# Kernel optimization log

Measured on AMD Instinct MI355X. Metric: run time of the kernel, lower is better.

Reference implementation:

```python
import jax, jax.numpy as jnp
import numpy as np

B, S, D, H = 4, 2048, 1024, 16
DK = D // H


def setup_inputs() -> dict:
    key = jax.random.key(0)
    ks = jax.random.split(key, 9)
    sc = 1.0 / np.sqrt(D)
    return {
        "query": jax.random.normal(ks[0], (B, S, D), jnp.float32),
        "key": jax.random.normal(ks[1], (B, S, D), jnp.float32),
        "value": jax.random.normal(ks[2], (B, S, D), jnp.float32),
        "Wq": jax.random.normal(ks[3], (D, D), jnp.float32) * sc,
        "bq": jax.random.normal(ks[4], (D,), jnp.float32) * sc,
        "Wk": jax.random.normal(ks[5], (D, D), jnp.float32) * sc,
        "bk": jax.random.normal(ks[6], (D,), jnp.float32) * sc,
        "Wv": jax.random.normal(ks[7], (D, D), jnp.float32) * sc,
        "bv": jax.random.normal(ks[8], (D,), jnp.float32) * sc,
    }


def reference(query, key, value, Wq, bq, Wk, bk, Wv, bv):
    # QKV projections, split into heads: [B,S,D] -> [B,H,S,DK]
    q = (query @ Wq + bq).reshape(B, S, H, DK).transpose(0, 2, 1, 3)
    k = (key @ Wk + bk).reshape(B, S, H, DK).transpose(0, 2, 1, 3)
    v = (value @ Wv + bv).reshape(B, S, H, DK).transpose(0, 2, 1, 3)
    # NOTE: original module applies NO 1/sqrt(d_k) scaling
    attn = jnp.einsum("bhqd,bhkd->bhqk", q, k)
    attn = jax.nn.softmax(attn, axis=-1)  # dropout is identity at inference
    ctx = jnp.einsum("bhqk,bhkd->bhqd", attn, v)
    ctx = ctx.transpose(0, 2, 1, 3).reshape(B, S, D)
    # original adds residual to raw concatenated context (no output projection)
    return ctx + query
```

## Files before the change

### kernel.cpp

```cpp
#include <hip/hip_runtime.h>
#include <hip/hip_bf16.h>
#include <stdint.h>

#define Bb 4
#define Ss 2048
#define Dd 1024
#define Hh 16
#define DK 64
#define BH 64
#define Mm 8192
#define KVT 64

typedef __attribute__((ext_vector_type(8))) _Float16 f16x8;
typedef __attribute__((ext_vector_type(4))) _Float16 f16x4;
typedef __attribute__((ext_vector_type(2))) __fp16 fp16x2;
typedef __attribute__((ext_vector_type(4))) float f32x4;
typedef __attribute__((ext_vector_type(16))) float f32x16;
typedef __attribute__((ext_vector_type(2))) unsigned uint2v;

__device__ __forceinline__ void gload16(const _Float16* g, _Float16* lds) {
  __builtin_amdgcn_global_load_lds((const __attribute__((address_space(1))) unsigned int*)g,
                                   (__attribute__((address_space(3))) unsigned int*)lds, 16, 0, 0);
}

#if __has_builtin(__builtin_amdgcn_exp2f)
__device__ __forceinline__ float ex2(float x) { return __builtin_amdgcn_exp2f(x); }
#else
__device__ __forceinline__ float ex2(float x) {
  float r; asm("v_exp_f32 %0, %1" : "=v"(r) : "v"(x)); return r;
}
#endif

__device__ __forceinline__ unsigned pk2u(float a, float b) {
  union { fp16x2 h; unsigned u; } x;
  x.h = __builtin_amdgcn_cvt_pkrtz(a, b);
  return x.u;
}

__device__ __forceinline__ float xhalf_max(float x) {
  union { float f; unsigned u; } a; a.f = x;
  uint2v r = __builtin_amdgcn_permlane32_swap(a.u, a.u, false, false);
  union { unsigned u; float f; } b0, b1; b0.u = r[0]; b1.u = r[1];
  return fmaxf(fmaxf(x, b0.f), b1.f);
}

__global__ __launch_bounds__(256) void cvt_wt(const float* __restrict__ wq,
                                              const float* __restrict__ wk,
                                              const float* __restrict__ wv,
                                              _Float16* __restrict__ tq,
                                              _Float16* __restrict__ tk,
                                              _Float16* __restrict__ tv) {
  const float* w = blockIdx.z == 0 ? wq : (blockIdx.z == 1 ? wk : wv);
  _Float16* o = blockIdx.z == 0 ? tq : (blockIdx.z == 1 ? tk : tv);
  float wscale = blockIdx.z == 0 ? 1.4426950408889634f : 1.0f;
  __shared__ float tile[64][65];
  int k0 = blockIdx.x * 64;
  int n0 = blockIdx.y * 64;
  int t = threadIdx.x;
  int tr = t >> 4;
  int tc = (t & 15) * 4;
  for (int i = 0; i < 4; i++) {
    int r = i * 16 + tr;
    float4 val = *(const float4*)(w + (k0 + r) * Dd + n0 + tc);
    tile[r][tc + 0] = val.x; tile[r][tc + 1] = val.y;
    tile[r][tc + 2] = val.z; tile[r][tc + 3] = val.w;
  }
  __syncthreads();
  for (int i = 0; i < 2; i++) {
    int vdx = t + 256 * i;
    int rn = vdx >> 3;
    int c8 = (vdx & 7) * 8;
    union { f16x8 v8; _Float16 h[8]; } o2;
    for (int j = 0; j < 8; j++) o2.h[j] = (_Float16)(tile[c8 + j][rn] * wscale);
    *(f16x8*)(o + (n0 + rn) * Dd + k0 + c8) = o2.v8;
  }
}

__global__ __launch_bounds__(256) void gemm_qkv(
    const float* __restrict__ aq, const float* __restrict__ ak,
    const float* __restrict__ av,
    const _Float16* __restrict__ wtq, const _Float16* __restrict__ wtk,
    const _Float16* __restrict__ wtv,
    const float* __restrict__ bq, const float* __restrict__ bk, const float* __restrict__ bv,
    _Float16* __restrict__ oq, _Float16* __restrict__ ok,
    _Float16* __restrict__ ov) {
  int z = blockIdx.z;
  const float* Af    = z == 0 ? aq  : (z == 1 ? ak  : av);
  const _Float16* Bt = z == 0 ? wtq : (z == 1 ? wtk : wtv);
  const float* bias  = z == 0 ? bq  : (z == 1 ? bk  : bv);
  _Float16* out      = z == 0 ? oq  : (z == 1 ? ok  : ov);
  float bscale       = z == 0 ? 1.4426950408889634f : 1.0f;

  __shared__ _Float16 As[2][128 * 64];
  __shared__ _Float16 Bs[2][128 * 64];

  int tid = threadIdx.x;
  int w = tid >> 6;
  int l = tid & 63;
  int lr = l & 15, lk = l >> 4;
  int m0 = blockIdx.x * 128;
  int n0 = blockIdx.y * 128;
  int wr = (w >> 1) * 64;
  int wc = (w & 1) * 64;

  int srow = l >> 3;
  int cs = (l & 7) ^ srow;
  const float*    ap[4];
  const _Float16* bp[4];
#pragma unroll
  for (int i = 0; i < 4; i++) {
    int row = i * 32 + w * 8 + srow;
    ap[i] = Af + (size_t)(m0 + row) * Dd + cs * 8;
    bp[i] = Bt + (size_t)(n0 + row) * Dd + cs * 8;
  }

  f32x4 acc[4][4] = {};
  int lr7 = lr & 7;
  int rs0 = (lk ^ lr7) * 8;
  int rs1 = ((4 + lk) ^ lr7) * 8;

#define ALOAD(AR)                                                         \
  _Pragma("unroll")                                                       \
  for (int i = 0; i < 4; i++) {                                           \
    AR[i][0] = *(const float4*)(ap[i]);                                   \
    AR[i][1] = *(const float4*)(ap[i] + 4);                               \
    ap[i] += 64;                                                          \
  }
#define BDMA(NXT)                                                         \
  _Pragma("unroll")                                                       \
  for (int i = 0; i < 4; i++) {                                           \
    gload16(bp[i], &Bs[NXT][(i * 256 + w * 64) * 8]);                     \
    bp[i] += 64;                                                          \
  }
#define AWRITE(AR, NXT)                                                   \
  _Pragma("unroll")                                                       \
  for (int i = 0; i < 4; i++) {                                           \
    union { unsigned u[4]; f16x8 v; } aw;                                 \
    aw.u[0] = pk2u(AR[i][0].x, AR[i][0].y);                               \
    aw.u[1] = pk2u(AR[i][0].z, AR[i][0].w);                               \
    aw.u[2] = pk2u(AR[i][1].x, AR[i][1].y);                               \
    aw.u[3] = pk2u(AR[i][1].z, AR[i][1].w);                               \
    *(f16x8*)&As[NXT][(i * 256 + w * 64 + l) * 8] = aw.v;                 \
  }
#define GCOMP(CUR)                                                              \
  _Pragma("unroll")                                                             \
  for (int kh = 0; kh < 2; kh++) {                                              \
    int rs = kh ? rs1 : rs0;                                                    \
    f16x8 af[4], bf[4];                                                         \
    _Pragma("unroll")                                                           \
    for (int mi = 0; mi < 4; mi++)                                              \
      af[mi] = *(const f16x8*)&As[CUR][(wr + mi * 16 + lr) * 64 + rs];          \
    _Pragma("unroll")                                                           \
    for (int ni = 0; ni < 4; ni++)                                              \
      bf[ni] = *(const f16x8*)&Bs[CUR][(wc + ni * 16 + lr) * 64 + rs];          \
    _Pragma("unroll")                                                           \
    for (int mi = 0; mi < 4; mi++)                                              \
      _Pragma("unroll")                                                         \
      for (int ni = 0; ni < 4; ni++)                                            \
        acc[mi][ni] = __builtin_amdgcn_mfma_f32_16x16x32_f16(af[mi], bf[ni], acc[mi][ni], 0, 0, 0); \
  }

  {
    float4 ar[4][2];
    ALOAD(ar)
    BDMA(0)
    AWRITE(ar, 0)
  }
  __syncthreads();

  for (int it = 0; it < 7; ++it) {
    {
      float4 ar[4][2];
      ALOAD(ar)
      BDMA(1)
      GCOMP(0)
      AWRITE(ar, 1)
    }
    __syncthreads();
    {
      float4 ar[4][2];
      ALOAD(ar)
      BDMA(0)
      GCOMP(1)
      AWRITE(ar, 0)
    }
    __syncthreads();
  }
  {
    float4 ar[4][2];
    ALOAD(ar)
    BDMA(1)
    GCOMP(0)
    AWRITE(ar, 1)
  }
  __syncthreads();
  GCOMP(1)
#undef GCOMP
#undef AWRITE
#undef BDMA
#undef ALOAD

  if (z == 2) {
    for (int mi = 0; mi < 4; mi++) {
      for (int ni = 0; ni < 4; ni++) {
        int n = n0 + wc + ni * 16 + lr;
        float bval = bias[n];
        int h = n >> 6, dk = n & 63;
        int m = m0 + wr + mi * 16 + lk * 4;
        int b = m >> 11, s = m & 2047;
        f16x4 o4;
        for (int j = 0; j < 4; j++) o4[j] = (_Float16)(acc[mi][ni][j] + bval);
        *(f16x4*)(out + ((size_t)((b * Hh + h) * DK + dk) * Ss + s)) = o4;
      }
    }
  } else {
    for (int mi = 0; mi < 4; mi++) {
      for (int ni = 0; ni < 4; ni++) {
        int n = n0 + wc + ni * 16 + lr;
        float bval = bias[n] * bscale;
        int h = n >> 6, dk = n & 63;
        for (int j = 0; j < 4; j++) {
          int m = m0 + wr + mi * 16 + lk * 4 + j;
          int b = m >> 11, s = m & 2047;
          out[((b * Hh + h) * Ss + s) * DK + dk] = (_Float16)(acc[mi][ni][j] + bval);
        }
      }
    }
  }
}

__global__ __launch_bounds__(256) void attn(const _Float16* __restrict__ Qb,
                                            const _Float16* __restrict__ Kb,
                                            const _Float16* __restrict__ Vt,
                                            const float* __restrict__ query,
                                            float* __restrict__ outp) {
  __shared__ _Float16 Kl[2][KVT * 64];
  __shared__ _Float16 Vl[2][KVT * 64];

  int tid = threadIdx.x;
  int w = tid >> 6, l = tid & 63;
  int l31 = l & 31, hi = l >> 5;
  int bh = blockIdx.x;
  int q0 = blockIdx.y * 128 + w * 32;
  const _Float16* Qp = Qb + bh * (Ss * DK);
  const _Float16* Kp = Kb + bh * (Ss * DK);
  const _Float16* Vp = Vt + bh * (DK * Ss);

  int srow = l >> 3;
  int sslot = (l & 7) ^ (srow & 7);
  int w16 = w * 16;
  const _Float16* kp0 = Kp + (w16 + srow) * DK + sslot * 8;
  const _Float16* kp1 = Kp + (w16 + 8 + srow) * DK + sslot * 8;
  const _Float16* vp0 = Vp + (w16 + srow) * Ss + sslot * 8;
  const _Float16* vp1 = Vp + (w16 + 8 + srow) * Ss + sslot * 8;

#define STAGE(BUF)                                                        \
  {                                                                       \
    gload16(kp0, &Kl[BUF][w16 * 64]);                                     \
    gload16(kp1, &Kl[BUF][(w16 + 8) * 64]);                               \
    gload16(vp0, &Vl[BUF][w16 * 64]);                                     \
    gload16(vp1, &Vl[BUF][(w16 + 8) * 64]);                               \
    kp0 += KVT * DK; kp1 += KVT * DK; vp0 += KVT; vp1 += KVT;             \
  }

  f16x8 qf[4];
#pragma unroll
  for (int s = 0; s < 4; s++)
    qf[s] = *(const f16x8*)(Qp + (q0 + l31) * DK + s * 16 + hi * 8);

  f32x16 o0 = {}, o1 = {};
  float mrun = -1e30f, lrun = 0.f;

  int kv7 = l31 & 7;
  int rslot[4];
#pragma unroll
  for (int s = 0; s < 4; s++) rslot[s] = ((s * 2 + hi) ^ kv7) * 8;

#define TILE(BUF)                                                               \
  {                                                                             \
    f32x16 s0 = {}, s1 = {};                                                    \
    _Pragma("unroll")                                                           \
    for (int s = 0; s < 4; s++) {                                               \
      f16x8 ka = *(const f16x8*)&Kl[BUF][l31 * 64 + rslot[s]];                  \
      s0 = __builtin_amdgcn_mfma_f32_32x32x16_f16(ka, qf[s], s0, 0, 0, 0);      \
    }                                                                           \
    _Pragma("unroll")                                                           \
    for (int s = 0; s < 4; s++) {                                               \
      f16x8 kb = *(const f16x8*)&Kl[BUF][(32 + l31) * 64 + rslot[s]];           \
      s1 = __builtin_amdgcn_mfma_f32_32x32x16_f16(kb, qf[s], s1, 0, 0, 0);      \
    }                                                                           \
    float m8[8];                                                                \
    _Pragma("unroll")                                                           \
    for (int r = 0; r < 8; r++)                                                 \
      m8[r] = fmaxf(fmaxf(s0[r], s0[r + 8]), fmaxf(s1[r], s1[r + 8]));          \
    _Pragma("unroll")                                                           \
    for (int d = 4; d >= 1; d >>= 1)                                            \
      for (int r = 0; r < 4; r++) if (r < d) m8[r] = fmaxf(m8[r], m8[r + d]);   \
    float pm = xhalf_max(m8[0]);                                                \
    if (!__all(pm - mrun <= 8.f)) {            \
      float mn = fmaxf(mrun, pm);                                               \
      float sc_ = ex2(mrun - mn);                                               \
      mrun = mn;                                                                \
      lrun *= sc_;                                                              \
      _Pragma("unroll")                                                         \
      for (int r = 0; r < 16; r++) { o0[r] *= sc_; o1[r] *= sc_; }              \
    }                                                                           \
    _Pragma("unroll")                                                           \
    for (int r = 0; r < 16; r++) {                                              \
      s0[r] = ex2(s0[r] - mrun);                                                \
      s1[r] = ex2(s1[r] - mrun);                                                \
    }                                                                           \
    float s8[8];                                                                \
    _Pragma("unroll")                                                           \
    for (int r = 0; r < 8; r++) s8[r] = (s0[r] + s0[r + 8]) + (s1[r] + s1[r + 8]); \
    _Pragma("unroll")                                                           \
    for (int d = 4; d >= 1; d >>= 1)                                            \
      for (int r = 0; r < 4; r++) if (r < d) s8[r] += s8[r + d];                \
    lrun += s8[0];                                                              \
    PVSTEP(BUF, s0, 0, 0)                                                       \
    PVSTEP(BUF, s0, 8, 1)                                                       \
    PVSTEP(BUF, s1, 0, 2)                                                       \
    PVSTEP(BUF, s1, 8, 3)                                                       \
  }

#define PVSTEP(BUF, SRC, OFF, KST)                                              \
    {                                                                           \
      unsigned a0 = pk2u(SRC[(OFF) + 0], SRC[(OFF) + 1]);                       \
      unsigned a1 = pk2u(SRC[(OFF) + 2], SRC[(OFF) + 3]);                       \
      unsigned b0 = pk2u(SRC[(OFF) + 4], SRC[(OFF) + 5]);                       \
      unsigned b1 = pk2u(SRC[(OFF) + 6], SRC[(OFF) + 7]);                       \
      uint2v r0 = __builtin_amdgcn_permlane32_swap(a0, b0, false, false);       \
      uint2v r1 = __builtin_amdgcn_permlane32_swap(a1, b1, false, false);       \
      union { unsigned u[4]; f16x8 v; } pf;                                     \
      pf.u[0] = r0[0]; pf.u[1] = r1[0]; pf.u[2] = r0[1]; pf.u[3] = r1[1];       \
      f16x8 v0 = *(const f16x8*)&Vl[BUF][l31 * 64 + rslot[KST]];                \
      f16x8 v1 = *(const f16x8*)&Vl[BUF][(32 + l31) * 64 + rslot[KST]];         \
      o0 = __builtin_amdgcn_mfma_f32_32x32x16_f16(v0, pf.v, o0, 0, 0, 0);       \
      o1 = __builtin_amdgcn_mfma_f32_32x32x16_f16(v1, pf.v, o1, 0, 0, 0);       \
    }

  STAGE(0)
  __syncthreads();

  for (int it = 0; it < 15; ++it) {
    STAGE(1)
    TILE(0)
    __syncthreads();
    STAGE(0)
    TILE(1)
    __syncthreads();
  }
  STAGE(1)
  TILE(0)
  __syncthreads();
  TILE(1)
#undef PVSTEP
#undef TILE
#undef STAGE

  lrun += __shfl_xor(lrun, 32);
  int b = bh >> 4, h = bh & 15;
  float inv = 1.f / lrun;
  int base = (b * Ss + q0 + l31) * Dd + h * 64;
#pragma unroll
  for (int rq = 0; rq < 4; rq++) {
    int d0 = rq * 8 + hi * 4;
    float4 qv0 = *(const float4*)(query + base + d0);
    float4 ov0;
    ov0.x = o0[rq * 4 + 0] * inv + qv0.x;
    ov0.y = o0[rq * 4 + 1] * inv + qv0.y;
    ov0.z = o0[rq * 4 + 2] * inv + qv0.z;
    ov0.w = o0[rq * 4 + 3] * inv + qv0.w;
    *(float4*)(outp + base + d0) = ov0;
    float4 qv1 = *(const float4*)(query + base + 32 + d0);
    float4 ov1;
    ov1.x = o1[rq * 4 + 0] * inv + qv1.x;
    ov1.y = o1[rq * 4 + 1] * inv + qv1.y;
    ov1.z = o1[rq * 4 + 2] * inv + qv1.z;
    ov1.w = o1[rq * 4 + 3] * inv + qv1.w;
    *(float4*)(outp + base + 32 + d0) = ov1;
  }
}

extern "C" void kernel_launch(void* const* d_in, const int* in_sizes, int n_in,
                              void* d_out, int out_size, void* d_ws, size_t ws_size,
                              hipStream_t stream) {
  const float* query = (const float*)d_in[0];
  const float* key   = (const float*)d_in[1];
  const float* value = (const float*)d_in[2];
  const float* Wq = (const float*)d_in[3];
  const float* bq = (const float*)d_in[4];
  const float* Wk = (const float*)d_in[5];
  const float* bk = (const float*)d_in[6];
  const float* Wv = (const float*)d_in[7];
  const float* bv = (const float*)d_in[8];
  float* out = (float*)d_out;

  _Float16* ws = (_Float16*)d_ws;
  const size_t ACT = (size_t)Mm * Dd;
  const size_t WSZ = (size_t)Dd * Dd;
  _Float16* Wtq  = ws;
  _Float16* Wtk  = Wtq + WSZ;
  _Float16* Wtv  = Wtk + WSZ;
  _Float16* Qb   = Wtv + WSZ;
  _Float16* Kb   = Qb + ACT;
  _Float16* VtT  = Kb + ACT;

  cvt_wt<<<dim3(16, 16, 3), dim3(256), 0, stream>>>(Wq, Wk, Wv, Wtq, Wtk, Wtv);
  gemm_qkv<<<dim3(64, 8, 3), dim3(256), 0, stream>>>(query, key, value, Wtq, Wtk, Wtv,
                                                     bq, bk, bv, Qb, Kb, VtT);
  attn<<<dim3(64, 16), dim3(256), 0, stream>>>(Qb, Kb, VtT, query, out);
}
```

Baseline: 195.4 us.

## Restructure attention into single-wave blocks with vmcnt-based double buffering

The attention kernel now runs one wave per block on 32 query rows and streams 32-key K/V tiles into double-buffered LDS. Each wave loads its own tiles, so the block-wide barriers give way to explicit s_waitcnt vmcnt waits. s_setprio is raised around the MFMA sections. This drops cross-wave synchronisation, but each wave now loads all of K/V alone, with no sharing across four waves, so global/L2 traffic for K/V roughly quadruples and occupancy depends on many small blocks.

After: 230.1 us. +17.8%, slower.

```diff
diff --git a/kernel.cpp b/kernel.cpp
--- a/kernel.cpp
+++ b/kernel.cpp
@@ -9,7 +9,6 @@
 #define DK 64
 #define BH 64
 #define Mm 8192
-#define KVT 64
 
 typedef __attribute__((ext_vector_type(8))) _Float16 f16x8;
 typedef __attribute__((ext_vector_type(4))) _Float16 f16x4;
@@ -43,6 +42,12 @@
   union { unsigned u; float f; } b0, b1; b0.u = r[0]; b1.u = r[1];
   return fmaxf(fmaxf(x, b0.f), b1.f);
 }
+
+#define VW(N)                                                           \
+  do {                                                                  \
+    asm volatile("s_waitcnt vmcnt(" #N ")" ::: "memory");               \
+    __builtin_amdgcn_sched_barrier(0);                                  \
+  } while (0)
 
 __global__ __launch_bounds__(256) void cvt_wt(const float* __restrict__ wq,
                                               const float* __restrict__ wk,
@@ -229,38 +234,43 @@
   }
 }
 
-__global__ __launch_bounds__(256) void attn(const _Float16* __restrict__ Qb,
-                                            const _Float16* __restrict__ Kb,
-                                            const _Float16* __restrict__ Vt,
-                                            const float* __restrict__ query,
-                                            float* __restrict__ outp) {
-  __shared__ _Float16 Kl[2][KVT * 64];
-  __shared__ _Float16 Vl[2][KVT * 64];
-
-  int tid = threadIdx.x;
-  int w = tid >> 6, l = tid & 63;
+__global__ __launch_bounds__(64) void attn(const _Float16* __restrict__ Qb,
+                                           const _Float16* __restrict__ Kb,
+                                           const _Float16* __restrict__ Vt,
+                                           const float* __restrict__ query,
+                                           float* __restrict__ outp) {
+  __shared__ _Float16 Kl[2][32 * 64];
+  __shared__ _Float16 Vl[2][64 * 32];
+
+  int l = threadIdx.x;
   int l31 = l & 31, hi = l >> 5;
   int bh = blockIdx.x;
-  int q0 = blockIdx.y * 128 + w * 32;
+  int q0 = blockIdx.y * 32;
   const _Float16* Qp = Qb + bh * (Ss * DK);
   const _Float16* Kp = Kb + bh * (Ss * DK);
   const _Float16* Vp = Vt + bh * (DK * Ss);
 
-  int srow = l >> 3;
-  int sslot = (l & 7) ^ (srow & 7);
-  int w16 = w * 16;
-  const _Float16* kp0 = Kp + (w16 + srow) * DK + sslot * 8;
-  const _Float16* kp1 = Kp + (w16 + 8 + srow) * DK + sslot * 8;
-  const _Float16* vp0 = Vp + (w16 + srow) * Ss + sslot * 8;
-  const _Float16* vp1 = Vp + (w16 + 8 + srow) * Ss + sslot * 8;
-
-#define STAGE(BUF)                                                        \
+  int kr = l >> 3;
+  int kcs = (l & 7) ^ kr;
+  const _Float16* kpA = Kp + (kr + 0)  * DK + kcs * 8;
+  const _Float16* kpB = Kp + (kr + 8)  * DK + kcs * 8;
+  const _Float16* kpC = Kp + (kr + 16) * DK + kcs * 8;
+  const _Float16* kpD = Kp + (kr + 24) * DK + kcs * 8;
+  int vr = l >> 2;
+  int vcs = (l & 3) ^ ((l >> 3) & 3);
+  const _Float16* vpA = Vp + (vr + 0)  * Ss + vcs * 8;
+  const _Float16* vpB = Vp + (vr + 16) * Ss + vcs * 8;
+  const _Float16* vpC = Vp + (vr + 32) * Ss + vcs * 8;
+  const _Float16* vpD = Vp + (vr + 48) * Ss + vcs * 8;
+
+#define STAGE(B)                                                          \
   {                                                                       \
-    gload16(kp0, &Kl[BUF][w16 * 64]);                                     \
-    gload16(kp1, &Kl[BUF][(w16 + 8) * 64]);                               \
-    gload16(vp0, &Vl[BUF][w16 * 64]);                                     \
-    gload16(vp1, &Vl[BUF][(w16 + 8) * 64]);                               \
-    kp0 += KVT * DK; kp1 += KVT * DK; vp0 += KVT; vp1 += KVT;             \
+    gload16(kpA, &Kl[B][0 * 512]); gload16(kpB, &Kl[B][1 * 512]);         \
+    gload16(kpC, &Kl[B][2 * 512]); gload16(kpD, &Kl[B][3 * 512]);         \
+    gload16(vpA, &Vl[B][0 * 512]); gload16(vpB, &Vl[B][1 * 512]);         \
+    gload16(vpC, &Vl[B][2 * 512]); gload16(vpD, &Vl[B][3 * 512]);         \
+    kpA += 32 * DK; kpB += 32 * DK; kpC += 32 * DK; kpD += 32 * DK;       \
+    vpA += 32; vpB += 32; vpC += 32; vpD += 32;                           \
   }
 
   f16x8 qf[4];
@@ -275,24 +285,39 @@
   int rslot[4];
 #pragma unroll
   for (int s = 0; s < 4; s++) rslot[s] = ((s * 2 + hi) ^ kv7) * 8;
-
-#define TILE(BUF)                                                               \
+  int vsw = (l31 >> 1) & 3;
+  int vslot0 = ((0 * 2 + hi) ^ vsw) * 8;
+  int vslot1 = ((1 * 2 + hi) ^ vsw) * 8;
+
+#define PVST(B, OFF, VSL)                                                       \
+    {                                                                           \
+      unsigned a0 = pk2u(s0[(OFF) + 0], s0[(OFF) + 1]);                         \
+      unsigned a1 = pk2u(s0[(OFF) + 2], s0[(OFF) + 3]);                         \
+      unsigned b0 = pk2u(s0[(OFF) + 4], s0[(OFF) + 5]);                         \
+      unsigned b1 = pk2u(s0[(OFF) + 6], s0[(OFF) + 7]);                         \
+      uint2v r0 = __builtin_amdgcn_permlane32_swap(a0, b0, false, false);       \
+      uint2v r1 = __builtin_amdgcn_permlane32_swap(a1, b1, false, false);       \
+      union { unsigned u[4]; f16x8 v; } pf;                                     \
+      pf.u[0] = r0[0]; pf.u[1] = r1[0]; pf.u[2] = r0[1]; pf.u[3] = r1[1];       \
+      f16x8 v0 = *(const f16x8*)&Vl[B][l31 * 32 + (VSL)];                       \
+      f16x8 v1 = *(const f16x8*)&Vl[B][(32 + l31) * 32 + (VSL)];                \
+      o0 = __builtin_amdgcn_mfma_f32_32x32x16_f16(v0, pf.v, o0, 0, 0, 0);       \
+      o1 = __builtin_amdgcn_mfma_f32_32x32x16_f16(v1, pf.v, o1, 0, 0, 0);       \
+    }
+
+#define TILE(B)                                                                 \
   {                                                                             \
-    f32x16 s0 = {}, s1 = {};                                                    \
+    f32x16 s0 = {};                                                             \
+    __builtin_amdgcn_s_setprio(1);                                              \
     _Pragma("unroll")                                                           \
     for (int s = 0; s < 4; s++) {                                               \
-      f16x8 ka = *(const f16x8*)&Kl[BUF][l31 * 64 + rslot[s]];                  \
+      f16x8 ka = *(const f16x8*)&Kl[B][l31 * 64 + rslot[s]];                    \
       s0 = __builtin_amdgcn_mfma_f32_32x32x16_f16(ka, qf[s], s0, 0, 0, 0);      \
     }                                                                           \
-    _Pragma("unroll")                                                           \
-    for (int s = 0; s < 4; s++) {                                               \
-      f16x8 kb = *(const f16x8*)&Kl[BUF][(32 + l31) * 64 + rslot[s]];           \
-      s1 = __builtin_amdgcn_mfma_f32_32x32x16_f16(kb, qf[s], s1, 0, 0, 0);      \
-    }                                                                           \
+    __builtin_amdgcn_s_setprio(0);                                              \
     float m8[8];                                                                \
     _Pragma("unroll")                                                           \
-    for (int r = 0; r < 8; r++)                                                 \
-      m8[r] = fmaxf(fmaxf(s0[r], s0[r + 8]), fmaxf(s1[r], s1[r + 8]));          \
+    for (int r = 0; r < 8; r++) m8[r] = fmaxf(s0[r], s0[r + 8]);                \
     _Pragma("unroll")                                                           \
     for (int d = 4; d >= 1; d >>= 1)                                            \
       for (int r = 0; r < 4; r++) if (r < d) m8[r] = fmaxf(m8[r], m8[r + d]);   \
@@ -306,56 +331,37 @@
       for (int r = 0; r < 16; r++) { o0[r] *= sc_; o1[r] *= sc_; }              \
     }                                                                           \
     _Pragma("unroll")                                                           \
-    for (int r = 0; r < 16; r++) {                                              \
-      s0[r] = ex2(s0[r] - mrun);                                                \
-      s1[r] = ex2(s1[r] - mrun);                                                \
-    }                                                                           \
+    for (int r = 0; r < 16; r++) s0[r] = ex2(s0[r] - mrun);                     \
     float s8[8];                                                                \
     _Pragma("unroll")                                                           \
-    for (int r = 0; r < 8; r++) s8[r] = (s0[r] + s0[r + 8]) + (s1[r] + s1[r + 8]); \
+    for (int r = 0; r < 8; r++) s8[r] = s0[r] + s0[r + 8];                      \
     _Pragma("unroll")                                                           \
     for (int d = 4; d >= 1; d >>= 1)                                            \
       for (int r = 0; r < 4; r++) if (r < d) s8[r] += s8[r + d];                \
     lrun += s8[0];                                                              \
-    PVSTEP(BUF, s0, 0, 0)                                                       \
-    PVSTEP(BUF, s0, 8, 1)                                                       \
-    PVSTEP(BUF, s1, 0, 2)                                                       \
-    PVSTEP(BUF, s1, 8, 3)                                                       \
-  }
-
-#define PVSTEP(BUF, SRC, OFF, KST)                                              \
-    {                                                                           \
-      unsigned a0 = pk2u(SRC[(OFF) + 0], SRC[(OFF) + 1]);                       \
-      unsigned a1 = pk2u(SRC[(OFF) + 2], SRC[(OFF) + 3]);                       \
-      unsigned b0 = pk2u(SRC[(OFF) + 4], SRC[(OFF) + 5]);                       \
-      unsigned b1 = pk2u(SRC[(OFF) + 6], SRC[(OFF) + 7]);                       \
-      uint2v r0 = __builtin_amdgcn_permlane32_swap(a0, b0, false, false);       \
-      uint2v r1 = __builtin_amdgcn_permlane32_swap(a1, b1, false, false);       \
-      union { unsigned u[4]; f16x8 v; } pf;                                     \
-      pf.u[0] = r0[0]; pf.u[1] = r1[0]; pf.u[2] = r0[1]; pf.u[3] = r1[1];       \
-      f16x8 v0 = *(const f16x8*)&Vl[BUF][l31 * 64 + rslot[KST]];                \
-      f16x8 v1 = *(const f16x8*)&Vl[BUF][(32 + l31) * 64 + rslot[KST]];         \
-      o0 = __builtin_amdgcn_mfma_f32_32x32x16_f16(v0, pf.v, o0, 0, 0, 0);       \
-      o1 = __builtin_amdgcn_mfma_f32_32x32x16_f16(v1, pf.v, o1, 0, 0, 0);       \
-    }
+    __builtin_amdgcn_s_setprio(1);                                              \
+    PVST(B, 0, vslot0)                                                          \
+    PVST(B, 8, vslot1)                                                          \
+    __builtin_amdgcn_s_setprio(0);                                              \
+  }
 
   STAGE(0)
-  __syncthreads();
-
-  for (int it = 0; it < 15; ++it) {
+  STAGE(1)
+  VW(8);
+
+  for (int it = 0; it < 31; ++it) {
+    TILE(0)
+    STAGE(0)
+    VW(8);
+    TILE(1)
     STAGE(1)
-    TILE(0)
-    __syncthreads();
-    STAGE(0)
-    TILE(1)
-    __syncthreads();
-  }
-  STAGE(1)
+    VW(8);
+  }
   TILE(0)
-  __syncthreads();
+  VW(0);
   TILE(1)
-#undef PVSTEP
 #undef TILE
+#undef PVST
 #undef STAGE
 
   lrun += __shfl_xor(lrun, 32);
@@ -409,5 +415,5 @@
   cvt_wt<<<dim3(16, 16, 3), dim3(256), 0, stream>>>(Wq, Wk, Wv, Wtq, Wtk, Wtv);
   gemm_qkv<<<dim3(64, 8, 3), dim3(256), 0, stream>>>(query, key, value, Wtq, Wtk, Wtv,
                                                      bq, bk, bv, Qb, Kb, VtT);
-  attn<<<dim3(64, 16), dim3(256), 0, stream>>>(Qb, Kb, VtT, query, out);
-}
+  attn<<<dim3(64, 64), dim3(64), 0, stream>>>(Qb, Kb, VtT, query, out);
+}
```
